# Performance work log

Measured on AMD Instinct MI355X. Metric: run time of the kernel, lower is better.

Reference implementation:

```python
import jax, jax.numpy as jnp
import numpy as np

B, S, H, E, D, K = 2, 4096, 1024, 8, 2048, 2


def setup_inputs() -> dict:
    key = jax.random.key(0)
    ks = jax.random.split(key, 6)
    scale = 0.02
    return {
        "x": jax.random.normal(ks[0], (B, S, H), dtype=jnp.float32),
        "gate_w": jax.random.normal(ks[1], (E, H), dtype=jnp.float32) * scale,
        "w1": jax.random.normal(ks[2], (E, H, D), dtype=jnp.float32) * scale,
        "b1": jnp.zeros((E, D), dtype=jnp.float32),
        "w2": jax.random.normal(ks[3], (E, D, H), dtype=jnp.float32) * scale,
        "b2": jnp.zeros((E, H), dtype=jnp.float32),
    }


def reference(x, gate_w, w1, b1, w2, b2):
    b, s, h = x.shape
    e = gate_w.shape[0]
    # Router
    router_logits = jnp.einsum('bsh,eh->bse', x, gate_w)
    router_probs = jax.nn.softmax(router_logits, axis=-1)
    top_k_probs, expert_idx = jax.lax.top_k(router_probs, K)      # [B,S,K]
    top_k_probs = top_k_probs / top_k_probs.sum(axis=-1, keepdims=True)
    # Aux load-balancing loss (faithful to source: mean over batch only -> [S,E])
    oh = jax.nn.one_hot(expert_idx, e, dtype=x.dtype)             # [B,S,K,E]
    tokens_per_expert = oh.sum(axis=-2).mean(axis=0)              # [S,E]
    avg_prob = router_probs.mean(axis=(0, 1))                     # [E]
    aux_loss = e * (tokens_per_expert * avg_prob).sum()
    # Dense combine weights per token per expert: [B*S, E]
    combine = (oh * top_k_probs[..., None]).sum(axis=-2).reshape(-1, e)
    # Expert MLPs, batched over experts (grouped GEMM form)
    xf = x.reshape(-1, h)                                         # [T,H]
    hid = jax.nn.gelu(jnp.einsum('th,ehd->etd', xf, w1) + b1[:, None, :],
                      approximate=False)                          # [E,T,D]
    y = jnp.einsum('etd,edh->eth', hid, w2) + b2[:, None, :]      # [E,T,H]
    out = jnp.einsum('te,eth->th', combine, y)                    # [T,H]
    return out.reshape(b, s, h), aux_loss
```

## Files before the change

### kernel.cpp

```cpp
#include <hip/hip_runtime.h>
#include <hip/hip_bf16.h>
#include <math.h>

#define Bdim 2
#define Sdim 4096
#define Hdim 1024
#define Edim 8
#define Ddim 2048
#define Tdim (Bdim*Sdim)

typedef __attribute__((ext_vector_type(8))) __bf16 bfv8;
typedef __attribute__((ext_vector_type(8))) short s16x8;
typedef __attribute__((ext_vector_type(4))) short s16x4;
typedef __attribute__((ext_vector_type(4))) float f32x4;

__device__ __forceinline__ short f2bf(float f) {
    union { float f; unsigned u; } a; a.f = f;
    unsigned r = (a.u + 0x7fffu + ((a.u >> 16) & 1u)) >> 16;
    return (short)r;
}
__device__ __forceinline__ float bf2f(short s) {
    union { unsigned u; float f; } a; a.u = ((unsigned)(unsigned short)s) << 16;
    return a.f;
}
__device__ __forceinline__ float fgelu(float x) {
    float u = fminf(x * (1.5957691f + 0.07135481f * x * x), 60.0f);
    float t = __expf(u);
    return x * t / (t + 1.0f);
}

typedef const __attribute__((address_space(1))) unsigned int ga_u32;
typedef __attribute__((address_space(3))) unsigned int la_u32;

__device__ __forceinline__ void gl_lds16(const void* g, void* l) {
    __builtin_amdgcn_global_load_lds((ga_u32*)g, (la_u32*)l, 16, 0, 0);
}

#define G_RD(SLOT) do {                                                              \
    _Pragma("unroll") for (int n = 0; n < 4; ++n)                                    \
        bf[n] = *(const bfv8*)(lds + 32768 + (SLOT) * 8192 + offB[n]);               \
    _Pragma("unroll") for (int m = 0; m < 8; ++m)                                    \
        af[m] = *(const bfv8*)(lds + (SLOT) * 8192 + offA[m]);                       \
    __builtin_amdgcn_sched_barrier(0);                                               \
} while (0)

#define G_MM() do {                                                                  \
    __builtin_amdgcn_s_setprio(1);                                                   \
    _Pragma("unroll") for (int m = 0; m < 8; ++m)                                    \
        _Pragma("unroll") for (int n = 0; n < 4; ++n)                                \
            acc[m][n] = __builtin_amdgcn_mfma_f32_16x16x32_bf16(af[m], bf[n], acc[m][n], 0, 0, 0); \
    __builtin_amdgcn_s_setprio(0);                                                   \
    __builtin_amdgcn_sched_barrier(0);                                               \
} while (0)

#define G_PH(SRD, SST) do {                                                          \
    G_RD(SRD);                                                                       \
    stage(SST);                                                                      \
    asm volatile("s_waitcnt vmcnt(4)" ::: "memory");                                 \
    __builtin_amdgcn_s_barrier();                                                    \
    __builtin_amdgcn_sched_barrier(0);                                               \
    G_MM();                                                                          \
} while (0)

#define G_PH_VM0(SRD) do {                                                           \
    G_RD(SRD);                                                                       \
    asm volatile("s_waitcnt vmcnt(0)" ::: "memory");                                 \
    __builtin_amdgcn_s_barrier();                                                    \
    __builtin_amdgcn_sched_barrier(0);                                               \
    G_MM();                                                                          \
} while (0)

#define G_PH_LAST(SRD) do {                                                          \
    G_RD(SRD);                                                                       \
    G_MM();                                                                          \
} while (0)

__global__ __launch_bounds__(256) void router_kernel(
    const float* __restrict__ x, const float* __restrict__ gw,
    int* __restrict__ cnt, float* __restrict__ psum,
    int* __restrict__ ltok, float* __restrict__ lw,
    short* __restrict__ xb)
{
    __shared__ float gws[Edim * Hdim];
    __shared__ int   lcnt[Edim], gbase[Edim];
    __shared__ int   s_e[32], s_pos[32], s_tok[32];
    __shared__ float s_w[32];
    __shared__ float s_ps[4][8];

    int tid = threadIdx.x;
    for (int i = tid; i < Edim * Hdim / 4; i += 256)
        ((float4*)gws)[i] = ((const float4*)gw)[i];
    if (tid < Edim) lcnt[tid] = 0;
    __syncthreads();

    int wave = tid >> 6, lane = tid & 63;
    float ps = 0.f;

    for (int i = 0; i < 4; ++i) {
        int t = blockIdx.x * 16 + wave * 4 + i;
        double acc[Edim];
#pragma unroll
        for (int e = 0; e < Edim; ++e) acc[e] = 0.0;
#pragma unroll
        for (int kq = 0; kq < 4; ++kq) {
            float4 xv = *(const float4*)(x + (size_t)t * Hdim + kq * 256 + lane * 4);
            if (xb) {
                s16x4 h; h[0]=f2bf(xv.x); h[1]=f2bf(xv.y); h[2]=f2bf(xv.z); h[3]=f2bf(xv.w);
                *(s16x4*)(xb + (size_t)t * Hdim + kq * 256 + lane * 4) = h;
            }
#pragma unroll
            for (int e = 0; e < Edim; ++e) {
                float4 wv = *(const float4*)(&gws[e * Hdim + kq * 256 + lane * 4]);
                acc[e] += (double)xv.x * wv.x + (double)xv.y * wv.y
                        + (double)xv.z * wv.z + (double)xv.w * wv.w;
            }
        }
#pragma unroll
        for (int e = 0; e < Edim; ++e) {
            acc[e] += __shfl_xor(acc[e], 1, 64);
            acc[e] += __shfl_xor(acc[e], 2, 64);
            acc[e] += __shfl_xor(acc[e], 4, 64);
        }
        int el = lane & 7;
        double v = acc[0];
#pragma unroll
        for (int e = 1; e < Edim; ++e) if (el == e) v = acc[e];
        v += __shfl_xor(v, 8, 64);
        v += __shfl_xor(v, 16, 64);
        v += __shfl_xor(v, 32, 64);
        double mx = v;
        mx = fmax(mx, __shfl_xor(mx, 1, 64));
        mx = fmax(mx, __shfl_xor(mx, 2, 64));
        mx = fmax(mx, __shfl_xor(mx, 4, 64));
        float ex = __expf((float)(v - mx));
        float sm = ex;
        sm += __shfl_xor(sm, 1, 64);
        sm += __shfl_xor(sm, 2, 64);
        sm += __shfl_xor(sm, 4, 64);
        ps += ex / sm;
        double le[8];
#pragma unroll
        for (int e = 0; e < 8; ++e) le[e] = __shfl(v, e, 8);
        if (lane == 0) {
            int e1 = 0;
#pragma unroll
            for (int e = 1; e < 8; ++e) if (le[e] > le[e1]) e1 = e;
            int e2 = -1;
#pragma unroll
            for (int e = 0; e < 8; ++e) {
                if (e == e1) continue;
                if (e2 < 0 || le[e] > le[e2]) e2 = e;
            }
            float r = __expf((float)(le[e2] - le[e1]));
            float w1v = 1.0f / (1.0f + r);
            int lt = (wave * 4 + i) * 2;
            int p1 = atomicAdd(&lcnt[e1], 1);
            s_e[lt] = e1; s_pos[lt] = p1; s_tok[lt] = 2*t;     s_w[lt] = w1v;
            int p2 = atomicAdd(&lcnt[e2], 1);
            s_e[lt+1] = e2; s_pos[lt+1] = p2; s_tok[lt+1] = 2*t+1; s_w[lt+1] = 1.0f - w1v;
        }
    }
    if (lane < 8) s_ps[wave][lane] = ps;
    __syncthreads();
    if (tid < 8) {
        atomicAdd(&psum[tid], s_ps[0][tid] + s_ps[1][tid] + s_ps[2][tid] + s_ps[3][tid]);
        gbase[tid] = atomicAdd(&cnt[tid], lcnt[tid]);
    }
    __syncthreads();
    if (tid < 32) {
        int e = s_e[tid];
        int pos = gbase[e] + s_pos[tid];
        ltok[e * Tdim + pos] = s_tok[tid];
        lw[e * Tdim + pos] = s_w[tid];
    }
}

__global__ void aux_kernel(const int* __restrict__ cnt,
                           const float* __restrict__ psum,
                           int* __restrict__ eoff,
                           float* __restrict__ out_aux)
{
    if (threadIdx.x == 0 && blockIdx.x == 0) {
        double s = 0.0;
        int run = 0;
        for (int e = 0; e < Edim; ++e) {
            eoff[e] = run;
            run += cnt[e];
            s += ((double)cnt[e] / (double)Bdim) * ((double)psum[e] / (double)Tdim);
        }
        out_aux[0] = (float)((double)Edim * s);
    }
}

__global__ __launch_bounds__(256) void convt_kernel(const float* __restrict__ w,
                                                    short* __restrict__ wt, int R, int C)
{
    int e = blockIdx.z;
    int r0 = blockIdx.y * 64, c0 = blockIdx.x * 64;
    __shared__ short t[64][76];
    int tid = threadIdx.x;
    {
        int r = tid >> 2, cs = (tid & 3) * 16;
        const float* src = w + ((size_t)e * R + r0 + r) * C + c0 + cs;
#pragma unroll
        for (int q = 0; q < 4; ++q) {
            float4 v = *(const float4*)(src + q * 4);
            s16x4 h; h[0]=f2bf(v.x); h[1]=f2bf(v.y); h[2]=f2bf(v.z); h[3]=f2bf(v.w);
            *(s16x4*)(&t[r][cs + q * 4]) = h;
        }
    }
    __syncthreads();
    {
        int c = tid >> 2, rs = (tid & 3) * 16;
        short tmp[16];
#pragma unroll
        for (int j = 0; j < 16; ++j) tmp[j] = t[rs + j][c];
        short* dst = wt + ((size_t)e * C + c0 + c) * R + r0 + rs;
        *(s16x8*)dst = *(s16x8*)tmp;
        *(s16x8*)(dst + 8) = *(s16x8*)(tmp + 8);
    }
}


__global__ __launch_bounds__(512, 2) void gemm1n_kernel(
    const short* __restrict__ xb, const short* __restrict__ w1t,
    const float* __restrict__ b1, const int* __restrict__ cnt,
    const int* __restrict__ eoff, const int* __restrict__ ltok,
    short* __restrict__ hid)
{
    constexpr int GXN = Ddim / 256;
    int id = blockIdx.x;
    int e = id & 7;
    unsigned rem = (unsigned)id >> 3;
    int bx = rem & (GXN - 1);
    int by = rem / GXN;

    int n_e = cnt[e];
    int row0 = by * 256;
    if (row0 >= n_e) return;
    int col0 = bx * 256;
    int slot0 = eoff[e];

    __shared__ short lds[65536];
    char* ldsb = (char*)lds;

    int tid = threadIdx.x;
    int w = tid >> 6, lane = tid & 63;

    const short* aS[2]; const short* bS[2];
    int oD[2];
#pragma unroll
    for (int j = 0; j < 2; ++j) {
        int o = tid * 16 + j * 8192;
        oD[j] = o;
        int eff = o ^ (((o >> 7) & 7) << 4);
        int row = ((eff >> 7) << 1) | ((eff >> 6) & 1);
        int kB  = eff & 63;
        int gr = row0 + row; if (gr > n_e - 1) gr = n_e - 1;
        int tok = ltok[(size_t)e * Tdim + gr] >> 1;
        aS[j] = xb + (size_t)tok * Hdim + (kB >> 1);
        bS[j] = w1t + ((size_t)e * Ddim + col0 + row) * Hdim + (kB >> 1);
    }

    int fr = lane & 15, kg = lane >> 4;
    int wm = (w >> 2) * 128, wn = (w & 3) * 64;

    int offA[8], offB[4];
#pragma unroll
    for (int m = 0; m < 8; ++m) {
        int r = wm + m * 16 + fr;
        offA[m] = (r >> 1) * 64 + ((((r & 1) * 32) + kg * 8) ^ (((r >> 1) & 7) << 3));
    }
#pragma unroll
    for (int n = 0; n < 4; ++n) {
        int r = wn + n * 16 + fr;
        offB[n] = (r >> 1) * 64 + ((((r & 1) * 32) + kg * 8) ^ (((r >> 1) & 7) << 3));
    }

    f32x4 acc[8][4];
#pragma unroll
    for (int m = 0; m < 8; ++m)
#pragma unroll
        for (int n = 0; n < 4; ++n) acc[m][n] = (f32x4)0.0f;

    bfv8 af[8], bf[4];

    auto stage = [&](int s) {
#pragma unroll
        for (int j = 0; j < 2; ++j) {
            gl_lds16(aS[j], ldsb + s * 16384 + oD[j]);
            aS[j] += 32;
            gl_lds16(bS[j], ldsb + 65536 + s * 16384 + oD[j]);
            bS[j] += 32;
        }
    };

    constexpr int NH = Hdim / 32;
    stage(0); stage(1);
    asm volatile("s_waitcnt vmcnt(4)" ::: "memory");
    __builtin_amdgcn_s_barrier();
    __builtin_amdgcn_sched_barrier(0);
#pragma unroll 1
    for (int it = 0; it < (NH - 4) / 4; ++it) {
        G_PH(0, 2); G_PH(1, 3); G_PH(2, 0); G_PH(3, 1);
    }
    G_PH(0, 2); G_PH(1, 3);
    G_PH_VM0(2);
    G_PH_LAST(3);

#pragma unroll
    for (int m = 0; m < 8; ++m) {
        int r0r = wm + m * 16 + kg * 4;
#pragma unroll
        for (int j = 0; j < 4; ++j) {
            int gr = row0 + r0r + j;
            if (gr >= n_e) continue;
            size_t hbase = (size_t)(slot0 + gr) * Ddim;
#pragma unroll
            for (int n = 0; n < 4; ++n) {
                int col = col0 + wn + n * 16 + fr;
                float v = acc[m][n][j] + b1[e * Ddim + col];
                hid[hbase + col] = f2bf(fgelu(v));
            }
        }
    }
}

__global__ __launch_bounds__(512, 2) void gemm2n_kernel(
    const short* __restrict__ hid, const short* __restrict__ w2t,
    const float* __restrict__ b2, const int* __restrict__ cnt,
    const int* __restrict__ eoff, const int* __restrict__ ltok,
    const float* __restrict__ lw, short* __restrict__ out2)
{
    constexpr int GXN = Hdim / 256;
    int id = blockIdx.x;
    int e = id & 7;
    unsigned rem = (unsigned)id >> 3;
    int bx = rem & (GXN - 1);
    int by = rem / GXN;

    int n_e = cnt[e];
    int row0 = by * 256;
    if (row0 >= n_e) return;
    int col0 = bx * 256;
    int slot0 = eoff[e];

    __shared__ short lds[65536];
    char* ldsb = (char*)lds;

    int tid = threadIdx.x;
    int w = tid >> 6, lane = tid & 63;

    const short* aS[2]; const short* bS[2];
    int oD[2];
#pragma unroll
    for (int j = 0; j < 2; ++j) {
        int o = tid * 16 + j * 8192;
        oD[j] = o;
        int eff = o ^ (((o >> 7) & 7) << 4);
        int row = ((eff >> 7) << 1) | ((eff >> 6) & 1);
        int kB  = eff & 63;
        int gr = row0 + row; if (gr > n_e - 1) gr = n_e - 1;
        aS[j] = hid + (size_t)(slot0 + gr) * Ddim + (kB >> 1);
        bS[j] = w2t + ((size_t)e * Hdim + col0 + row) * Ddim + (kB >> 1);
    }

    int fr = lane & 15, kg = lane >> 4;
    int wm = (w >> 2) * 128, wn = (w & 3) * 64;

    int offA[8], offB[4];
#pragma unroll
    for (int m = 0; m < 8; ++m) {
        int r = wm + m * 16 + fr;
        offA[m] = (r >> 1) * 64 + ((((r & 1) * 32) + kg * 8) ^ (((r >> 1) & 7) << 3));
    }
#pragma unroll
    for (int n = 0; n < 4; ++n) {
        int r = wn + n * 16 + fr;
        offB[n] = (r >> 1) * 64 + ((((r & 1) * 32) + kg * 8) ^ (((r >> 1) & 7) << 3));
    }

    f32x4 acc[8][4];
#pragma unroll
    for (int m = 0; m < 8; ++m)
#pragma unroll
        for (int n = 0; n < 4; ++n) acc[m][n] = (f32x4)0.0f;

    bfv8 af[8], bf[4];

    auto stage = [&](int s) {
#pragma unroll
        for (int j = 0; j < 2; ++j) {
            gl_lds16(aS[j], ldsb + s * 16384 + oD[j]);
            aS[j] += 32;
            gl_lds16(bS[j], ldsb + 65536 + s * 16384 + oD[j]);
            bS[j] += 32;
        }
    };

    constexpr int NH = Ddim / 32;
    stage(0); stage(1);
    asm volatile("s_waitcnt vmcnt(4)" ::: "memory");
    __builtin_amdgcn_s_barrier();
    __builtin_amdgcn_sched_barrier(0);
#pragma unroll 1
    for (int it = 0; it < (NH - 4) / 4; ++it) {
        G_PH(0, 2); G_PH(1, 3); G_PH(2, 0); G_PH(3, 1);
    }
    G_PH(0, 2); G_PH(1, 3);
    G_PH_VM0(2);
    G_PH_LAST(3);

#pragma unroll
    for (int m = 0; m < 8; ++m) {
        int r0r = wm + m * 16 + kg * 4;
#pragma unroll
        for (int j = 0; j < 4; ++j) {
            int gr = row0 + r0r + j;
            if (gr >= n_e) continue;
            int val = ltok[(size_t)e * Tdim + gr];
            float p = lw[(size_t)e * Tdim + gr];
            size_t obase = (size_t)val * Hdim;
#pragma unroll
            for (int n = 0; n < 4; ++n) {
                int col = col0 + wn + n * 16 + fr;
                float v = p * (acc[m][n][j] + b2[e * Hdim + col]);
                out2[obase + col] = f2bf(v);
            }
        }
    }
}

__global__ __launch_bounds__(256) void combine_kernel(const short* __restrict__ out2,
                                                      float* __restrict__ out)
{
    size_t i = ((size_t)blockIdx.x * 256 + threadIdx.x) * 8;
    size_t t = i >> 10;
    int h = (int)(i & 1023);
    s16x8 a = *(const s16x8*)(out2 + (t * 2) * 1024 + h);
    s16x8 b = *(const s16x8*)(out2 + (t * 2 + 1) * 1024 + h);
    float4 o0, o1;
    o0.x = bf2f(a[0]) + bf2f(b[0]); o0.y = bf2f(a[1]) + bf2f(b[1]);
    o0.z = bf2f(a[2]) + bf2f(b[2]); o0.w = bf2f(a[3]) + bf2f(b[3]);
    o1.x = bf2f(a[4]) + bf2f(b[4]); o1.y = bf2f(a[5]) + bf2f(b[5]);
    o1.z = bf2f(a[6]) + bf2f(b[6]); o1.w = bf2f(a[7]) + bf2f(b[7]);
    *(float4*)(out + i) = o0;
    *(float4*)(out + i + 4) = o1;
}

#define FBK 64
#define FLDK 72

__global__ __launch_bounds__(256) void gemm1_fb(
    const float* __restrict__ x, const float* __restrict__ w1,
    const float* __restrict__ b1, const int* __restrict__ cnt,
    const int* __restrict__ ltok, short* __restrict__ hid,
    int CH, int row_base)
{
    int e = blockIdx.z;
    int n_e = cnt[e];
    int row0 = row_base + blockIdx.y * 128;
    if (row0 >= n_e) return;
    int col0 = blockIdx.x * 128;

    __shared__ short As[128][FLDK];
    __shared__ short Bs[128][FLDK];

    int tid = threadIdx.x;
    int arow = tid >> 1;
    int akh  = (tid & 1) * 32;
    int gr_a = row0 + arow;
    int tok = ltok[(size_t)e * Tdim + (gr_a < n_e ? gr_a : n_e - 1)] >> 1;
    const float* xrow = x + (size_t)tok * Hdim + akh;
    int bdg = (tid & 31) * 4;
    int bkg = (tid >> 5) * 4;

    int lane = tid & 63;
    int wid = tid >> 6;
    int wm = (wid >> 1) * 64, wn = (wid & 1) * 64;
    int fr = lane & 15, kg = lane >> 4;

    f32x4 acc[4][4];
#pragma unroll
    for (int m = 0; m < 4; ++m)
#pragma unroll
        for (int n = 0; n < 4; ++n) acc[m][n] = (f32x4)0.0f;

    const float* wB = w1 + (size_t)e * Hdim * Ddim + col0;

    for (int k0 = 0; k0 < Hdim; k0 += FBK) {
#pragma unroll
        for (int i = 0; i < 8; ++i) {
            float4 v = *(const float4*)(xrow + k0 + i * 4);
            s16x4 h; h[0] = f2bf(v.x); h[1] = f2bf(v.y); h[2] = f2bf(v.z); h[3] = f2bf(v.w);
            *(s16x4*)(&As[arow][akh + i * 4]) = h;
        }
#pragma unroll
        for (int r = 0; r < 2; ++r) {
            int kq = bkg + r * 32;
            float4 v0 = *(const float4*)(wB + (size_t)(k0 + kq + 0) * Ddim + bdg);
            float4 v1 = *(const float4*)(wB + (size_t)(k0 + kq + 1) * Ddim + bdg);
            float4 v2 = *(const float4*)(wB + (size_t)(k0 + kq + 2) * Ddim + bdg);
            float4 v3 = *(const float4*)(wB + (size_t)(k0 + kq + 3) * Ddim + bdg);
            const float* p0 = (const float*)&v0; const float* p1 = (const float*)&v1;
            const float* p2 = (const float*)&v2; const float* p3 = (const float*)&v3;
#pragma unroll
            for (int c = 0; c < 4; ++c) {
                s16x4 h; h[0] = f2bf(p0[c]); h[1] = f2bf(p1[c]); h[2] = f2bf(p2[c]); h[3] = f2bf(p3[c]);
                *(s16x4*)(&Bs[bdg + c][kq]) = h;
            }
        }
        __syncthreads();
        bfv8 af[4][2], bfr[4][2];
#pragma unroll
        for (int m = 0; m < 4; ++m)
#pragma unroll
            for (int kk = 0; kk < 2; ++kk)
                af[m][kk] = *(const bfv8*)(&As[wm + m * 16 + fr][kk * 32 + kg * 8]);
#pragma unroll
        for (int n = 0; n < 4; ++n)
#pragma unroll
            for (int kk = 0; kk < 2; ++kk)
                bfr[n][kk] = *(const bfv8*)(&Bs[wn + n * 16 + fr][kk * 32 + kg * 8]);
#pragma unroll
        for (int m = 0; m < 4; ++m)
#pragma unroll
            for (int n = 0; n < 4; ++n) {
                acc[m][n] = __builtin_amdgcn_mfma_f32_16x16x32_bf16(af[m][0], bfr[n][0], acc[m][n], 0, 0, 0);
                acc[m][n] = __builtin_amdgcn_mfma_f32_16x16x32_bf16(af[m][1], bfr[n][1], acc[m][n], 0, 0, 0);
            }
        __syncthreads();
    }

    int lr0 = row0 - row_base;
#pragma unroll
    for (int m = 0; m < 4; ++m) {
        int r0r = wm + m * 16 + kg * 4;
#pragma unroll
        for (int j = 0; j < 4; ++j) {
            int gr = row0 + r0r + j;
            if (gr >= n_e) continue;
            size_t hbase = ((size_t)e * CH + (size_t)(lr0 + r0r + j)) * Ddim;
#pragma unroll
            for (int n = 0; n < 4; ++n) {
                int col = col0 + wn + n * 16 + fr;
                float v = acc[m][n][j] + b1[e * Ddim + col];
                float g = 0.5f * v * (1.0f + erff(v * 0.70710678118654752440f));
                hid[hbase + col] = f2bf(g);
            }
        }
    }
}

__global__ __launch_bounds__(256) void gemm2_fb(
    const short* __restrict__ hid, const float* __restrict__ w2,
    const float* __restrict__ b2, const int* __restrict__ cnt,
    const int* __restrict__ ltok, const float* __restrict__ lw,
    float* __restrict__ out, int CH, int row_base)
{
    int e = blockIdx.z;
    int n_e = cnt[e];
    int row0 = row_base + blockIdx.y * 128;
    if (row0 >= n_e) return;
    int col0 = blockIdx.x * 128;

    __shared__ short As[128][FLDK];
    __shared__ short Bs[128][FLDK];

    int tid = threadIdx.x;
    int arow = tid >> 1;
    int akh  = (tid & 1) * 32;
    const short* hrow = hid + ((size_t)e * CH + (size_t)(row0 - row_base + arow)) * Ddim + akh;
    int bdg = (tid & 31) * 4;
    int bkg = (tid >> 5) * 4;

    int lane = tid & 63;
    int wid = tid >> 6;
    int wm = (wid >> 1) * 64, wn = (wid & 1) * 64;
    int fr = lane & 15, kg = lane >> 4;

    f32x4 acc[4][4];
#pragma unroll
    for (int m = 0; m < 4; ++m)
#pragma unroll
        for (int n = 0; n < 4; ++n) acc[m][n] = (f32x4)0.0f;

    const float* wB = w2 + (size_t)e * Ddim * Hdim + col0;

    for (int k0 = 0; k0 < Ddim; k0 += FBK) {
#pragma unroll
        for (int i = 0; i < 4; ++i) {
            s16x8 v = *(const s16x8*)(hrow + k0 + i * 8);
            *(s16x8*)(&As[arow][akh + i * 8]) = v;
        }
#pragma unroll
        for (int r = 0; r < 2; ++r) {
            int kq = bkg + r * 32;
            float4 v0 = *(const float4*)(wB + (size_t)(k0 + kq + 0) * Hdim + bdg);
            float4 v1 = *(const float4*)(wB + (size_t)(k0 + kq + 1) * Hdim + bdg);
            float4 v2 = *(const float4*)(wB + (size_t)(k0 + kq + 2) * Hdim + bdg);
            float4 v3 = *(const float4*)(wB + (size_t)(k0 + kq + 3) * Hdim + bdg);
            const float* p0 = (const float*)&v0; const float* p1 = (const float*)&v1;
            const float* p2 = (const float*)&v2; const float* p3 = (const float*)&v3;
#pragma unroll
            for (int c = 0; c < 4; ++c) {
                s16x4 h; h[0] = f2bf(p0[c]); h[1] = f2bf(p1[c]); h[2] = f2bf(p2[c]); h[3] = f2bf(p3[c]);
                *(s16x4*)(&Bs[bdg + c][kq]) = h;
            }
        }
        __syncthreads();
        bfv8 af[4][2], bfr[4][2];
#pragma unroll
        for (int m = 0; m < 4; ++m)
#pragma unroll
            for (int kk = 0; kk < 2; ++kk)
                af[m][kk] = *(const bfv8*)(&As[wm + m * 16 + fr][kk * 32 + kg * 8]);
#pragma unroll
        for (int n = 0; n < 4; ++n)
#pragma unroll
            for (int kk = 0; kk < 2; ++kk)
                bfr[n][kk] = *(const bfv8*)(&Bs[wn + n * 16 + fr][kk * 32 + kg * 8]);
#pragma unroll
        for (int m = 0; m < 4; ++m)
#pragma unroll
            for (int n = 0; n < 4; ++n) {
                acc[m][n] = __builtin_amdgcn_mfma_f32_16x16x32_bf16(af[m][0], bfr[n][0], acc[m][n], 0, 0, 0);
                acc[m][n] = __builtin_amdgcn_mfma_f32_16x16x32_bf16(af[m][1], bfr[n][1], acc[m][n], 0, 0, 0);
            }
        __syncthreads();
    }

#pragma unroll
    for (int m = 0; m < 4; ++m) {
        int r0r = wm + m * 16 + kg * 4;
#pragma unroll
        for (int j = 0; j < 4; ++j) {
            int gr = row0 + r0r + j;
            if (gr >= n_e) continue;
            int tok = ltok[(size_t)e * Tdim + gr] >> 1;
            float p = lw[(size_t)e * Tdim + gr];
#pragma unroll
            for (int n = 0; n < 4; ++n) {
                int col = col0 + wn + n * 16 + fr;
                float v = p * (acc[m][n][j] + b2[e * Hdim + col]);
                atomicAdd(&out[(size_t)tok * Hdim + col], v);
            }
        }
    }
}

extern "C" void kernel_launch(void* const* d_in, const int* in_sizes, int n_in,
                              void* d_out, int out_size, void* d_ws, size_t ws_size,
                              hipStream_t stream)
{
    const float* x  = (const float*)d_in[0];
    const float* gw = (const float*)d_in[1];
    const float* w1 = (const float*)d_in[2];
    const float* b1 = (const float*)d_in[3];
    const float* w2 = (const float*)d_in[4];
    const float* b2 = (const float*)d_in[5];
    float* out = (float*)d_out;

    char* wsb = (char*)d_ws;
    int*   cnt  = (int*)wsb;
    float* psum = (float*)(wsb + 32);
    int*   eoff = (int*)(wsb + 64);
    int*   ltok = (int*)(wsb + 128);
    float* lwp  = (float*)(wsb + 128 + (size_t)Edim * Tdim * 4);
    size_t lists_end = 128 + (size_t)Edim * Tdim * 8;

    size_t xb_sz = (size_t)Tdim * Hdim * 2;
    size_t w1t_sz = (size_t)Edim * Hdim * Ddim * 2;
    size_t w2t_sz = w1t_sz;
    size_t hid_sz = (size_t)(2 * Tdim) * Ddim * 2;
    size_t req = lists_end + xb_sz + w1t_sz + w2t_sz + hid_sz;

    hipMemsetAsync(wsb, 0, 128, stream);

    if (req <= ws_size) {
        short* xb   = (short*)(wsb + lists_end);
        short* w1t  = (short*)(wsb + lists_end + xb_sz);
        short* w2t  = (short*)(wsb + lists_end + xb_sz + w1t_sz);
        short* hid  = (short*)(wsb + lists_end + xb_sz + w1t_sz + w2t_sz);
        short* out2 = w1t;

        convt_kernel<<<dim3(Ddim / 64, Hdim / 64, Edim), 256, 0, stream>>>(w1, w1t, Hdim, Ddim);
        convt_kernel<<<dim3(Hdim / 64, Ddim / 64, Edim), 256, 0, stream>>>(w2, w2t, Ddim, Hdim);
        router_kernel<<<Tdim / 16, 256, 0, stream>>>(x, gw, cnt, psum, ltok, lwp, xb);
        aux_kernel<<<1, 64, 0, stream>>>(cnt, psum, eoff, out + (size_t)Tdim * Hdim);

        gemm1n_kernel<<<(Ddim / 256) * 32 * Edim, 512, 0, stream>>>(
            xb, w1t, b1, cnt, eoff, ltok, hid);
        gemm2n_kernel<<<(Hdim / 256) * 32 * Edim, 512, 0, stream>>>(
            hid, w2t, b2, cnt, eoff, ltok, lwp, out2);
        combine_kernel<<<(size_t)Tdim * Hdim / 2048, 256, 0, stream>>>(out2, out);
    } else {
        short* hid = (short*)(wsb + lists_end);
        int CH2 = 2048;
        while (CH2 > 128 && lists_end + (size_t)Edim * CH2 * Ddim * 2 > ws_size) CH2 >>= 1;

        hipMemsetAsync(d_out, 0, (size_t)out_size * 4, stream);
        router_kernel<<<Tdim / 16, 256, 0, stream>>>(x, gw, cnt, psum, ltok, lwp, nullptr);
        aux_kernel<<<1, 64, 0, stream>>>(cnt, psum, eoff, out + (size_t)Tdim * Hdim);

        int chunks = Tdim / CH2;
        for (int c = 0; c < chunks; ++c) {
            gemm1_fb<<<dim3(Ddim / 128, CH2 / 128, Edim), 256, 0, stream>>>(
                x, w1, b1, cnt, ltok, hid, CH2, c * CH2);
            gemm2_fb<<<dim3(Hdim / 128, CH2 / 128, Edim), 256, 0, stream>>>(
                hid, w2, b2, cnt, ltok, lwp, out, CH2, c * CH2);
        }
    }
}
```

Before: 337.0 us.

## Deepen GEMM prefetch to three stages and merge weight conversion kernels

Both expert GEMM kernels now prefetch three K-slices into the four-slot LDS ring instead of two, waiting on vmcnt(8) so more global loads stay in flight while MFMAs run. The epilogue phases are rewritten to drain the deeper pipeline, and the waits now also cover lgkmcnt. The two weight transpose/convert launches are merged into one kernel that picks w1 or w2 from blockIdx.z, saving a launch. The deeper prefetch keeps more loads outstanding and changes the ring slot rotation, which risks ordering mistakes in the pipeline.

After: 328.5 us. 2.5% less time.

```diff
diff --git a/kernel.cpp b/kernel.cpp
--- a/kernel.cpp
+++ b/kernel.cpp
@@ -53,24 +53,32 @@
     __builtin_amdgcn_sched_barrier(0);                                               \
 } while (0)
 
-#define G_PH(SRD, SST) do {                                                          \
+#define PH_S(SRD, SST) do {                                                          \
     G_RD(SRD);                                                                       \
     stage(SST);                                                                      \
-    asm volatile("s_waitcnt vmcnt(4)" ::: "memory");                                 \
+    asm volatile("s_waitcnt vmcnt(8) lgkmcnt(0)" ::: "memory");                      \
     __builtin_amdgcn_s_barrier();                                                    \
     __builtin_amdgcn_sched_barrier(0);                                               \
     G_MM();                                                                          \
 } while (0)
 
-#define G_PH_VM0(SRD) do {                                                           \
+#define PH_T4(SRD) do {                                                              \
     G_RD(SRD);                                                                       \
-    asm volatile("s_waitcnt vmcnt(0)" ::: "memory");                                 \
+    asm volatile("s_waitcnt vmcnt(4) lgkmcnt(0)" ::: "memory");                      \
     __builtin_amdgcn_s_barrier();                                                    \
     __builtin_amdgcn_sched_barrier(0);                                               \
     G_MM();                                                                          \
 } while (0)
 
-#define G_PH_LAST(SRD) do {                                                          \
+#define PH_T0(SRD) do {                                                              \
+    G_RD(SRD);                                                                       \
+    asm volatile("s_waitcnt vmcnt(0) lgkmcnt(0)" ::: "memory");                      \
+    __builtin_amdgcn_s_barrier();                                                    \
+    __builtin_amdgcn_sched_barrier(0);                                               \
+    G_MM();                                                                          \
+} while (0)
+
+#define PH_TL(SRD) do {                                                              \
     G_RD(SRD);                                                                       \
     G_MM();                                                                          \
 } while (0)
@@ -192,11 +200,15 @@
     }
 }
 
-__global__ __launch_bounds__(256) void convt_kernel(const float* __restrict__ w,
-                                                    short* __restrict__ wt, int R, int C)
-{
-    int e = blockIdx.z;
-    int r0 = blockIdx.y * 64, c0 = blockIdx.x * 64;
+__global__ __launch_bounds__(256) void convt2_kernel(
+    const float* __restrict__ w1, const float* __restrict__ w2,
+    short* __restrict__ w1t, short* __restrict__ w2t)
+{
+    int z = blockIdx.z;
+    const float* w; short* wt; int R, C, r0, c0, e;
+    if (z < 8) { e = z;     w = w1; wt = w1t; R = Hdim; C = Ddim; r0 = blockIdx.y * 64; c0 = blockIdx.x * 64; }
+    else       { e = z - 8; w = w2; wt = w2t; R = Ddim; C = Hdim; r0 = blockIdx.x * 64; c0 = blockIdx.y * 64; }
+
     __shared__ short t[64][76];
     int tid = threadIdx.x;
     {
@@ -296,17 +308,18 @@
     };
 
     constexpr int NH = Hdim / 32;
-    stage(0); stage(1);
-    asm volatile("s_waitcnt vmcnt(4)" ::: "memory");
+    stage(0); stage(1); stage(2);
+    asm volatile("s_waitcnt vmcnt(8)" ::: "memory");
     __builtin_amdgcn_s_barrier();
     __builtin_amdgcn_sched_barrier(0);
 #pragma unroll 1
     for (int it = 0; it < (NH - 4) / 4; ++it) {
-        G_PH(0, 2); G_PH(1, 3); G_PH(2, 0); G_PH(3, 1);
-    }
-    G_PH(0, 2); G_PH(1, 3);
-    G_PH_VM0(2);
-    G_PH_LAST(3);
+        PH_S(0, 3); PH_S(1, 0); PH_S(2, 1); PH_S(3, 2);
+    }
+    PH_S(0, 3);
+    PH_T4(1);
+    PH_T0(2);
+    PH_TL(3);
 
 #pragma unroll
     for (int m = 0; m < 8; ++m) {
@@ -399,17 +412,18 @@
     };
 
     constexpr int NH = Ddim / 32;
-    stage(0); stage(1);
-    asm volatile("s_waitcnt vmcnt(4)" ::: "memory");
+    stage(0); stage(1); stage(2);
+    asm volatile("s_waitcnt vmcnt(8)" ::: "memory");
     __builtin_amdgcn_s_barrier();
     __builtin_amdgcn_sched_barrier(0);
 #pragma unroll 1
     for (int it = 0; it < (NH - 4) / 4; ++it) {
-        G_PH(0, 2); G_PH(1, 3); G_PH(2, 0); G_PH(3, 1);
-    }
-    G_PH(0, 2); G_PH(1, 3);
-    G_PH_VM0(2);
-    G_PH_LAST(3);
+        PH_S(0, 3); PH_S(1, 0); PH_S(2, 1); PH_S(3, 2);
+    }
+    PH_S(0, 3);
+    PH_T4(1);
+    PH_T0(2);
+    PH_TL(3);
 
 #pragma unroll
     for (int m = 0; m < 8; ++m) {
@@ -684,8 +698,7 @@
         short* hid  = (short*)(wsb + lists_end + xb_sz + w1t_sz + w2t_sz);
         short* out2 = w1t;
 
-        convt_kernel<<<dim3(Ddim / 64, Hdim / 64, Edim), 256, 0, stream>>>(w1, w1t, Hdim, Ddim);
-        convt_kernel<<<dim3(Hdim / 64, Ddim / 64, Edim), 256, 0, stream>>>(w2, w2t, Ddim, Hdim);
+        convt2_kernel<<<dim3(32, 16, 16), 256, 0, stream>>>(w1, w2, w1t, w2t);
         router_kernel<<<Tdim / 16, 256, 0, stream>>>(x, gw, cnt, psum, ltok, lwp, xb);
         aux_kernel<<<1, 64, 0, stream>>>(cnt, psum, eoff, out + (size_t)Tdim * Hdim);
 
```
